# Performance work log

Measured on AMD Instinct MI355X. Metric: run time of the kernel, lower is better.

The kernel has to match this reference:

```python
import jax, jax.numpy as jnp
import numpy as np

B, T, F, H = 64, 512, 1024, 1024

def setup_inputs() -> dict:
    key = jax.random.key(0)
    ks = jax.random.split(key, 13)
    def w(k, shape):
        return jax.random.normal(k, shape, dtype=jnp.float32) * 0.02
    inp = {"x": jax.random.normal(ks[0], (B, T, F), dtype=jnp.float32)}
    names = ["i", "f", "g", "o"]
    for j, n in enumerate(names):
        inp[f"U_{n}"] = w(ks[1 + 3 * j], (F, H))
        inp[f"V_{n}"] = w(ks[2 + 3 * j], (H, H))
        inp[f"b_{n}"] = w(ks[3 + 3 * j], (H,))
    return inp


def reference(x, U_i, V_i, b_i, U_f, V_f, b_f, U_g, V_g, b_g, U_o, V_o, b_o):
    batch = x.shape[0]
    hid = V_i.shape[0]
    # Concatenate the 4 gate projections into single GEMMs (same math, fused).
    U = jnp.concatenate([U_i, U_f, U_g, U_o], axis=1)  # [F, 4H]
    V = jnp.concatenate([V_i, V_f, V_g, V_o], axis=1)  # [H, 4H]
    b = jnp.concatenate([b_i, b_f, b_g, b_o], axis=0)  # [4H]
    # Precompute input contribution for all timesteps in one big GEMM.
    xU = jnp.einsum("btf,fk->btk", x, U) + b           # [B, T, 4H]
    xU_t = jnp.swapaxes(xU, 0, 1)                       # [T, B, 4H]

    def step(carry, xu):
        h, c = carry
        z = xu + h @ V                                  # [B, 4H]
        zi, zf, zg, zo = jnp.split(z, 4, axis=-1)
        i_t = jax.nn.sigmoid(zi)
        f_t = jax.nn.sigmoid(zf)
        g_t = jnp.tanh(zg)
        o_t = jnp.tanh(zo)  # NOTE: source uses tanh (not sigmoid) for output gate
        c = f_t * c + i_t * g_t
        h = o_t * jnp.tanh(c)
        return (h, c), None

    h0 = jnp.zeros((batch, hid), dtype=x.dtype)
    c0 = jnp.zeros((batch, hid), dtype=x.dtype)
    (h_t, c_t), _ = jax.lax.scan(step, (h0, c0), xU_t)
    return h_t
```

## Files before the change

### kernel.cpp

```cpp
#include <hip/hip_runtime.h>

using u16 = unsigned short;
using u32 = unsigned int;
using u64 = unsigned long long;
using bf16x8 = __attribute__((ext_vector_type(8))) short;
using f16x8  = __attribute__((ext_vector_type(8))) _Float16;
using f32x4  = __attribute__((ext_vector_type(4))) float;
using u32x4  = __attribute__((ext_vector_type(4))) unsigned int;

static constexpr size_t XU_OFF = 0;
static constexpr size_t XU_BYTES = (size_t)512 * 64 * 4096 * 2;
static constexpr size_t XB_OFF = XU_OFF + XU_BYTES;
static constexpr size_t XB_BYTES = (size_t)64 * 512 * 1024 * 2;
static constexpr size_t UT_OFF = XB_OFF + XB_BYTES;
static constexpr size_t WT_BYTES = (size_t)4096 * 1024 * 2;
static constexpr size_t VT_OFF = UT_OFF + WT_BYTES;
static constexpr size_t BP_OFF = VT_OFF + WT_BYTES;
static constexpr size_t BP_BYTES = 4096 * 4;
static constexpr size_t HT_PLANE = (size_t)2 * 4 * 16 * 1024 * 2;
static constexpr size_t HHI_OFF = BP_OFF + BP_BYTES;
static constexpr size_t HLO_OFF = HHI_OFF + HT_PLANE;
static constexpr size_t FLAG_OFF = HLO_OFF + HT_PLANE;
static constexpr size_t FLAG_BYTES = 4096;

__device__ __forceinline__ float bf2f(u32 u) {
    return __uint_as_float(u << 16);
}
__device__ __forceinline__ u16 f2bf(float f) {
    u32 u = __float_as_uint(f);
    u32 r = (u + 0x7FFFu + ((u >> 16) & 1u)) >> 16;
    return (u16)r;
}
__device__ __forceinline__ u16 f2h(float f) {
    _Float16 x = (_Float16)f;
    union { _Float16 h; u16 u; } cv;
    cv.h = x;
    return cv.u;
}

__device__ __forceinline__ float fast_sigmoid(float x) {
    return __builtin_amdgcn_rcpf(1.f + __expf(-x));
}
__device__ __forceinline__ float fast_tanh(float x) {
    return 1.f - 2.f * __builtin_amdgcn_rcpf(1.f + __expf(2.f * x));
}

__device__ __forceinline__ u32x4 load16_uc(const u16* p) {
    u32x4 v;
    asm volatile("global_load_dwordx4 %0, %1, off sc0 sc1"
                 : "=v"(v)
                 : "v"(p));
    return v;
}

__device__ __forceinline__ void wait_vm4(int j, u32x4& a) {
    switch (j) {
    case 0:  asm volatile("s_waitcnt vmcnt(3)" : "+v"(a)); break;
    case 1:  asm volatile("s_waitcnt vmcnt(2)" : "+v"(a)); break;
    case 2:  asm volatile("s_waitcnt vmcnt(1)" : "+v"(a)); break;
    default: asm volatile("s_waitcnt vmcnt(0)" : "+v"(a)); break;
    }
}

__device__ __forceinline__ void gld16(const u16* g, u16* l) {
    __builtin_amdgcn_global_load_lds((const __attribute__((address_space(1))) void*)g,
                                     (__attribute__((address_space(3))) void*)l,
                                     16, 0, 0);
}

__global__ void cvt_x_kernel(const float4* __restrict__ x, uint2* __restrict__ xb) {
    int i = blockIdx.x * 256 + threadIdx.x;
#pragma unroll
    for (int k = 0; k < 8; ++k) {
        int idx = i + k * 1048576;
        float4 v = x[idx];
        uint2 o;
        o.x = (u32)f2bf(v.x) | ((u32)f2bf(v.y) << 16);
        o.y = (u32)f2bf(v.z) | ((u32)f2bf(v.w) << 16);
        xb[idx] = o;
    }
}

__global__ void repack_kernel(const float* U0, const float* U1, const float* U2, const float* U3,
                              const float* V0, const float* V1, const float* V2, const float* V3,
                              u16* UT, u16* VT) {
    __shared__ u16 tile[64][65];
    int bx  = blockIdx.x;
    int mat = bx >> 8;
    int rem = bx & 255;
    int tf = rem >> 4, th = rem & 15;
    int f0 = tf * 64, h0 = th * 64;
    const float* srcs[8] = {U0, U1, U2, U3, V0, V1, V2, V3};
    const float* s = srcs[mat];
    u16* d = (mat < 4) ? UT : VT;
    bool isU = (mat < 4);
    int g = mat & 3;
    int c = threadIdx.x & 63;
    int r = threadIdx.x >> 6;
#pragma unroll
    for (int i = 0; i < 16; ++i) {
        int fr = r + i * 4;
        float v = s[(size_t)(f0 + fr) * 1024 + h0 + c];
        tile[fr][c] = isU ? f2bf(v) : f2h(v);
    }
    __syncthreads();
#pragma unroll
    for (int i = 0; i < 16; ++i) {
        int hcl = r + i * 4;
        d[(size_t)((h0 + hcl) * 4 + g) * 1024 + f0 + c] = tile[c][hcl];
    }
}

__global__ void bias_kernel(const float* b0, const float* b1, const float* b2, const float* b3,
                            float* bp) {
    int n = blockIdx.x * 256 + threadIdx.x;
    int g = n & 3, hc = n >> 2;
    const float* bs[4] = {b0, b1, b2, b3};
    bp[n] = bs[g][hc];
}

__global__ void __launch_bounds__(256) gemm_xu_kernel(const u16* __restrict__ xb,
                                                      const u16* __restrict__ UT,
                                                      const float* __restrict__ bp,
                                                      u16* __restrict__ xu) {
    __shared__ u16 As[128 * 32];
    __shared__ u16 Bs[128 * 32];

    int bx0 = blockIdx.x;
    int bx = (bx0 & 7) * 1024 + (bx0 >> 3);
    int nt = bx & 31, mt = bx >> 5;
    int tid = threadIdx.x;
    int lane = tid & 63, wv = tid >> 6;
    int wm = wv & 1, wn = wv >> 1;
    int l15 = lane & 15, quad = lane >> 4;

    int idr = tid >> 2, idk = (tid & 3) * 8;
    const u16* aSrc0 = xb + (size_t)(mt * 128 + idr) * 1024 + idk;
    const u16* aSrc1 = aSrc0 + (size_t)64 * 1024;
    const u16* bSrc0 = UT + (size_t)(nt * 128 + idr) * 1024 + idk;
    const u16* bSrc1 = bSrc0 + (size_t)64 * 1024;
    u16* aDst0 = As + (size_t)tid * 8;
    u16* aDst1 = As + (size_t)(tid + 256) * 8;
    u16* bDst0 = Bs + (size_t)tid * 8;
    u16* bDst1 = Bs + (size_t)(tid + 256) * 8;

    int arow = wm * 64 + l15;
    int brow = wn * 64 + l15;
    int brow0 = nt * 128 + brow;

    f32x4 acc[4][4];
#pragma unroll
    for (int i = 0; i < 4; ++i)
#pragma unroll
        for (int j = 0; j < 4; ++j) acc[i][j] = f32x4{0.f, 0.f, 0.f, 0.f};

    float biasv[4];
#pragma unroll
    for (int j = 0; j < 4; ++j) biasv[j] = bp[brow0 + 16 * j];

    for (int k0 = 0; k0 < 1024; k0 += 32) {
        gld16(aSrc0 + k0, aDst0);
        gld16(aSrc1 + k0, aDst1);
        gld16(bSrc0 + k0, bDst0);
        gld16(bSrc1 + k0, bDst1);
        __syncthreads();

        bf16x8 af[4], bfv[4];
#pragma unroll
        for (int i = 0; i < 4; ++i)
            af[i] = *(const bf16x8*)(As + (size_t)(arow + i * 16) * 32 + quad * 8);
#pragma unroll
        for (int j = 0; j < 4; ++j)
            bfv[j] = *(const bf16x8*)(Bs + (size_t)(brow + j * 16) * 32 + quad * 8);
#pragma unroll
        for (int i = 0; i < 4; ++i)
#pragma unroll
            for (int j = 0; j < 4; ++j)
                acc[i][j] = __builtin_amdgcn_mfma_f32_16x16x32_bf16(af[i], bfv[j], acc[i][j], 0, 0, 0);
        __syncthreads();
    }

#pragma unroll
    for (int i = 0; i < 4; ++i) {
        int rbase = mt * 128 + wm * 64 + 16 * i + quad * 4;
#pragma unroll
        for (int j = 0; j < 4; ++j) {
            int col = brow0 + 16 * j;
            float bj = biasv[j];
#pragma unroll
            for (int rg = 0; rg < 4; ++rg) {
                int r = rbase + rg;
                int b_i = r >> 9, t_i = r & 511;
                xu[((size_t)(t_i * 64 + b_i) << 12) + col] = f2bf(acc[i][j][rg] + bj);
            }
        }
    }
}

__global__ void __launch_bounds__(512, 2) lstm_rec_kernel(const u16* __restrict__ xu,
                                                          const u16* __restrict__ VT,
                                                          u16* hhi,
                                                          u16* hlo,
                                                          u32* flags,
                                                          float* __restrict__ out) {
    __shared__ float zs[8][16][132];

    int bx = blockIdx.x;
    int g  = bx & 3;
    int cb = bx >> 2;
    int tid = threadIdx.x;
    int lane = tid & 63, wv = tid >> 6;
    int l15 = lane & 15, quad = lane >> 4;
    int r  = tid >> 5;
    int hc = tid & 31;

    f16x8 vfrag[8][4];
    {
        const u16* vb = VT + ((size_t)(cb * 128 + l15) * 1024) + wv * 128 + quad * 8;
#pragma unroll
        for (int nt = 0; nt < 8; ++nt)
#pragma unroll
            for (int j = 0; j < 4; ++j)
                vfrag[nt][j] = *(const f16x8*)(vb + (size_t)nt * 16 * 1024 + j * 32);
    }

    u32* gflags = flags + g * 64;
    int myp = 4 * wv + (lane & 3);

    float c = 0.f;
    float h = 0.f;

    uint2 xraw = *(const uint2*)(xu + ((size_t)(g * 16 + r) << 12) + cb * 128 + hc * 4);

    for (int t = 0; t < 512; ++t) {
        f32x4 acc[8];
#pragma unroll
        for (int nt = 0; nt < 8; ++nt) acc[nt] = f32x4{0.f, 0.f, 0.f, 0.f};

        if (t) {
            for (;;) {
                u32 f = __hip_atomic_load(gflags + myp, __ATOMIC_RELAXED,
                                          __HIP_MEMORY_SCOPE_AGENT);
                if (__ballot(f >= (u32)t) == ~0ull) break;
                __builtin_amdgcn_s_sleep(1);
            }
            asm volatile("" ::: "memory");

            const u16* hB = hhi + (((size_t)(t & 1) * 4 + g) * 16 + l15) * 1024
                          + wv * 128 + quad * 8;
            u32x4 hv[4];
#pragma unroll
            for (int j = 0; j < 4; ++j)
                hv[j] = load16_uc(hB + j * 32);
#pragma unroll
            for (int j = 0; j < 4; ++j) {
                wait_vm4(j, hv[j]);
                union { u32x4 q; f16x8 v; } ah;
                ah.q = hv[j];
#pragma unroll
                for (int nt = 0; nt < 8; ++nt)
                    acc[nt] = __builtin_amdgcn_mfma_f32_16x16x32_f16(ah.v, vfrag[nt][j], acc[nt], 0, 0, 0);
            }
        }

#pragma unroll
        for (int nt = 0; nt < 8; ++nt)
#pragma unroll
            for (int rg = 0; rg < 4; ++rg)
                zs[wv][quad * 4 + rg][nt * 16 + l15] = acc[nt][rg];
        __syncthreads();

        float4 s = {0.f, 0.f, 0.f, 0.f};
#pragma unroll
        for (int w = 0; w < 8; ++w) {
            float4 v = *(const float4*)&zs[w][r][hc * 4];
            s.x += v.x; s.y += v.y; s.z += v.z; s.w += v.w;
        }
        float z0 = s.x + bf2f(xraw.x & 0xFFFFu);
        float z1 = s.y + bf2f(xraw.x >> 16);
        float z2 = s.z + bf2f(xraw.y & 0xFFFFu);
        float z3 = s.w + bf2f(xraw.y >> 16);

        float it_ = fast_sigmoid(z0);
        float ft_ = fast_sigmoid(z1);
        float gt_ = fast_tanh(z2);
        float ot_ = fast_tanh(z3);
        c = ft_ * c + it_ * gt_;
        h = ot_ * fast_tanh(c);

        if (t == 511) break;

        size_t sidx = (((size_t)((t + 1) & 1) * 4 + g) * 16 + r) * 1024 + cb * 32 + hc;
        __hip_atomic_store(hhi + sidx, f2h(h), __ATOMIC_RELAXED,
                           __HIP_MEMORY_SCOPE_AGENT);
        asm volatile("s_waitcnt vmcnt(0)" ::: "memory");
        __syncthreads();
        if (tid == 0)
            __hip_atomic_store(gflags + cb, (u32)(t + 1), __ATOMIC_RELAXED,
                               __HIP_MEMORY_SCOPE_AGENT);

        xraw = *(const uint2*)(xu + ((size_t)((t + 1) * 64 + g * 16 + r) << 12) + cb * 128 + hc * 4);
    }

    out[(size_t)(g * 16 + r) * 1024 + cb * 32 + hc] = h;
}

extern "C" void kernel_launch(void* const* d_in, const int* in_sizes, int n_in,
                              void* d_out, int out_size, void* d_ws, size_t ws_size,
                              hipStream_t stream) {
    char* ws = (char*)d_ws;
    const float* x = (const float*)d_in[0];
    const float *U[4], *V[4], *b[4];
    for (int g = 0; g < 4; ++g) {
        U[g] = (const float*)d_in[1 + 3 * g];
        V[g] = (const float*)d_in[2 + 3 * g];
        b[g] = (const float*)d_in[3 + 3 * g];
    }
    u16*   xu = (u16*)(ws + XU_OFF);
    u16*   xb = (u16*)(ws + XB_OFF);
    u16*   UT = (u16*)(ws + UT_OFF);
    u16*   VT = (u16*)(ws + VT_OFF);
    float* bp = (float*)(ws + BP_OFF);
    u16*   hhi = (u16*)(ws + HHI_OFF);
    u16*   hlo = (u16*)(ws + HLO_OFF);
    u32*   flags = (u32*)(ws + FLAG_OFF);
    float* out = (float*)d_out;

    hipMemsetAsync(ws + FLAG_OFF, 0, FLAG_BYTES, stream);

    cvt_x_kernel<<<4096, 256, 0, stream>>>((const float4*)x, (uint2*)xb);
    repack_kernel<<<2048, 256, 0, stream>>>(U[0], U[1], U[2], U[3],
                                            V[0], V[1], V[2], V[3], UT, VT);
    bias_kernel<<<16, 256, 0, stream>>>(b[0], b[1], b[2], b[3], bp);
    gemm_xu_kernel<<<8192, 256, 0, stream>>>(xb, UT, bp, xu);

    void* args[] = {(void*)&xu, (void*)&VT, (void*)&hhi, (void*)&hlo,
                    (void*)&flags, (void*)&out};
    hipLaunchCooperativeKernel((const void*)lstm_rec_kernel, dim3(128), dim3(512),
                               args, 0, stream);
}
```

Baseline: 2.222 ms.

## Fuse input-projection GEMM into recurrent kernel and overlap it with recurrence

Replaces the separate xU GEMM launch with a cooperative fused kernel of 256 blocks. Every block first computes 8 GEMM tiles, which covers the first time chunk. The 128 extra blocks then produce the remaining time chunks in the background while the 128 recurrent blocks consume them, gated by per-chunk atomic counters. GEMM output is staged through LDS and written with 16-byte write-through stores, and the unused hlo buffer is removed. The aim is to hide most of the GEMM behind the latency-bound recurrence. The risks are a smaller 128x64-per-wave-split GEMM tile, lower occupancy from the larger LDS footprint, and recurrent blocks stalling if producers fall behind.

```diff
diff --git a/kernel.cpp b/kernel.cpp
--- a/kernel.cpp
+++ b/kernel.cpp
@@ -19,8 +19,7 @@
 static constexpr size_t BP_BYTES = 4096 * 4;
 static constexpr size_t HT_PLANE = (size_t)2 * 4 * 16 * 1024 * 2;
 static constexpr size_t HHI_OFF = BP_OFF + BP_BYTES;
-static constexpr size_t HLO_OFF = HHI_OFF + HT_PLANE;
-static constexpr size_t FLAG_OFF = HLO_OFF + HT_PLANE;
+static constexpr size_t FLAG_OFF = HHI_OFF + HT_PLANE;
 static constexpr size_t FLAG_BYTES = 4096;
 
 __device__ __forceinline__ float bf2f(u32 u) {
@@ -53,6 +52,11 @@
     return v;
 }
 
+__device__ __forceinline__ void store16_wt(u16* p, u32x4 v) {
+    asm volatile("global_store_dwordx4 %0, %1, off sc0 sc1"
+                 :: "v"(p), "v"(v) : "memory");
+}
+
 __device__ __forceinline__ void wait_vm4(int j, u32x4& a) {
     switch (j) {
     case 0:  asm volatile("s_waitcnt vmcnt(3)" : "+v"(a)); break;
@@ -66,6 +70,15 @@
     __builtin_amdgcn_global_load_lds((const __attribute__((address_space(1))) void*)g,
                                      (__attribute__((address_space(3))) void*)l,
                                      16, 0, 0);
+}
+
+__device__ __forceinline__ void wait_chunk(const u32* cnt, int c) {
+    for (;;) {
+        u32 v = __hip_atomic_load(cnt + c, __ATOMIC_RELAXED, __HIP_MEMORY_SCOPE_AGENT);
+        if (v >= 2048u) break;
+        __builtin_amdgcn_s_sleep(8);
+    }
+    asm volatile("" ::: "memory");
 }
 
 __global__ void cvt_x_kernel(const float4* __restrict__ x, uint2* __restrict__ xb) {
@@ -119,93 +132,99 @@
     bp[n] = bs[g][hc];
 }
 
-__global__ void __launch_bounds__(256) gemm_xu_kernel(const u16* __restrict__ xb,
-                                                      const u16* __restrict__ UT,
-                                                      const float* __restrict__ bp,
-                                                      u16* __restrict__ xu) {
+__device__ __forceinline__ void gemm_tile(int tau,
+        const u16* __restrict__ xb, const u16* __restrict__ UT,
+        const float* __restrict__ bp, u16* __restrict__ xu,
+        u16* As, u16* Bs, u16* Cs, u32* cnt) {
+    int tc = tau >> 11, rem = tau & 2047;
+    int b = rem >> 5, nt = rem & 31, mt = b * 4 + tc;
+    int tid = threadIdx.x;
+    int lane = tid & 63, wv = tid >> 6;
+    int wm = wv >> 2, wn = wv & 3;
+    int l15 = lane & 15, quad = lane >> 4;
+
+    int idr = tid >> 2, idk = (tid & 3) * 8;
+    const u16* aS = xb + (size_t)(mt * 128 + idr) * 1024 + idk;
+    const u16* bS = UT + (size_t)(nt * 128 + idr) * 1024 + idk;
+    u16* aD = As + (size_t)tid * 8;
+    u16* bD = Bs + (size_t)tid * 8;
+
+    f32x4 acc[4][2];
+#pragma unroll
+    for (int i = 0; i < 4; ++i)
+#pragma unroll
+        for (int j = 0; j < 2; ++j) acc[i][j] = f32x4{0.f, 0.f, 0.f, 0.f};
+
+    float biasv[2];
+#pragma unroll
+    for (int j = 0; j < 2; ++j) biasv[j] = bp[nt * 128 + wn * 32 + j * 16 + l15];
+
+    for (int k0 = 0; k0 < 1024; k0 += 32) {
+        gld16(aS + k0, aD);
+        gld16(bS + k0, bD);
+        __syncthreads();
+        bf16x8 af[4], bfv[2];
+#pragma unroll
+        for (int i = 0; i < 4; ++i)
+            af[i] = *(const bf16x8*)(As + (size_t)(wm * 64 + i * 16 + l15) * 32 + quad * 8);
+#pragma unroll
+        for (int j = 0; j < 2; ++j)
+            bfv[j] = *(const bf16x8*)(Bs + (size_t)(wn * 32 + j * 16 + l15) * 32 + quad * 8);
+#pragma unroll
+        for (int i = 0; i < 4; ++i)
+#pragma unroll
+            for (int j = 0; j < 2; ++j)
+                acc[i][j] = __builtin_amdgcn_mfma_f32_16x16x32_bf16(af[i], bfv[j], acc[i][j], 0, 0, 0);
+        __syncthreads();
+    }
+
+#pragma unroll
+    for (int i = 0; i < 4; ++i)
+#pragma unroll
+        for (int j = 0; j < 2; ++j)
+#pragma unroll
+            for (int rg = 0; rg < 4; ++rg)
+                Cs[(size_t)(wm * 64 + i * 16 + quad * 4 + rg) * 136 + wn * 32 + j * 16 + l15] =
+                    f2bf(acc[i][j][rg] + biasv[j]);
+    __syncthreads();
+
+#pragma unroll
+    for (int p = 0; p < 4; ++p) {
+        int id = p * 512 + tid;
+        int row = id >> 4, q = id & 15;
+        u32x4 v = *(const u32x4*)(Cs + (size_t)row * 136 + q * 8);
+        int gr = mt * 128 + row;
+        int t_i = gr & 511, b_i = gr >> 9;
+        store16_wt(xu + (((size_t)(t_i * 64 + b_i)) << 12) + nt * 128 + q * 8, v);
+    }
+    asm volatile("s_waitcnt vmcnt(0)" ::: "memory");
+    __syncthreads();
+    if (tid == 0)
+        __hip_atomic_fetch_add(cnt + tc, 1u, __ATOMIC_RELAXED, __HIP_MEMORY_SCOPE_AGENT);
+}
+
+__global__ void __launch_bounds__(512, 2) lstm_fused_kernel(
+        const u16* __restrict__ xb, const u16* __restrict__ UT,
+        const float* __restrict__ bp, u16* __restrict__ xu,
+        const u16* __restrict__ VT, u16* hhi, u32* flags, u32* cnt,
+        float* __restrict__ out) {
     __shared__ u16 As[128 * 32];
     __shared__ u16 Bs[128 * 32];
-
-    int bx0 = blockIdx.x;
-    int bx = (bx0 & 7) * 1024 + (bx0 >> 3);
-    int nt = bx & 31, mt = bx >> 5;
-    int tid = threadIdx.x;
-    int lane = tid & 63, wv = tid >> 6;
-    int wm = wv & 1, wn = wv >> 1;
-    int l15 = lane & 15, quad = lane >> 4;
-
-    int idr = tid >> 2, idk = (tid & 3) * 8;
-    const u16* aSrc0 = xb + (size_t)(mt * 128 + idr) * 1024 + idk;
-    const u16* aSrc1 = aSrc0 + (size_t)64 * 1024;
-    const u16* bSrc0 = UT + (size_t)(nt * 128 + idr) * 1024 + idk;
-    const u16* bSrc1 = bSrc0 + (size_t)64 * 1024;
-    u16* aDst0 = As + (size_t)tid * 8;
-    u16* aDst1 = As + (size_t)(tid + 256) * 8;
-    u16* bDst0 = Bs + (size_t)tid * 8;
-    u16* bDst1 = Bs + (size_t)(tid + 256) * 8;
-
-    int arow = wm * 64 + l15;
-    int brow = wn * 64 + l15;
-    int brow0 = nt * 128 + brow;
-
-    f32x4 acc[4][4];
-#pragma unroll
-    for (int i = 0; i < 4; ++i)
-#pragma unroll
-        for (int j = 0; j < 4; ++j) acc[i][j] = f32x4{0.f, 0.f, 0.f, 0.f};
-
-    float biasv[4];
-#pragma unroll
-    for (int j = 0; j < 4; ++j) biasv[j] = bp[brow0 + 16 * j];
-
-    for (int k0 = 0; k0 < 1024; k0 += 32) {
-        gld16(aSrc0 + k0, aDst0);
-        gld16(aSrc1 + k0, aDst1);
-        gld16(bSrc0 + k0, bDst0);
-        gld16(bSrc1 + k0, bDst1);
-        __syncthreads();
-
-        bf16x8 af[4], bfv[4];
-#pragma unroll
-        for (int i = 0; i < 4; ++i)
-            af[i] = *(const bf16x8*)(As + (size_t)(arow + i * 16) * 32 + quad * 8);
-#pragma unroll
-        for (int j = 0; j < 4; ++j)
-            bfv[j] = *(const bf16x8*)(Bs + (size_t)(brow + j * 16) * 32 + quad * 8);
-#pragma unroll
-        for (int i = 0; i < 4; ++i)
-#pragma unroll
-            for (int j = 0; j < 4; ++j)
-                acc[i][j] = __builtin_amdgcn_mfma_f32_16x16x32_bf16(af[i], bfv[j], acc[i][j], 0, 0, 0);
-        __syncthreads();
-    }
-
-#pragma unroll
-    for (int i = 0; i < 4; ++i) {
-        int rbase = mt * 128 + wm * 64 + 16 * i + quad * 4;
-#pragma unroll
-        for (int j = 0; j < 4; ++j) {
-            int col = brow0 + 16 * j;
-            float bj = biasv[j];
-#pragma unroll
-            for (int rg = 0; rg < 4; ++rg) {
-                int r = rbase + rg;
-                int b_i = r >> 9, t_i = r & 511;
-                xu[((size_t)(t_i * 64 + b_i) << 12) + col] = f2bf(acc[i][j][rg] + bj);
-            }
-        }
-    }
-}
-
-__global__ void __launch_bounds__(512, 2) lstm_rec_kernel(const u16* __restrict__ xu,
-                                                          const u16* __restrict__ VT,
-                                                          u16* hhi,
-                                                          u16* hlo,
-                                                          u32* flags,
-                                                          float* __restrict__ out) {
+    __shared__ u16 Cs[128 * 136];
     __shared__ float zs[8][16][132];
 
     int bx = blockIdx.x;
+
+    for (int p = 0; p < 8; ++p)
+        gemm_tile(bx * 8 + p, xb, UT, bp, xu, As, Bs, Cs, cnt);
+
+    if (bx >= 128) {
+        int gid = bx - 128;
+        for (int p = 0; p < 48; ++p)
+            gemm_tile(2048 + p * 128 + gid, xb, UT, bp, xu, As, Bs, Cs, cnt);
+        return;
+    }
+
     int g  = bx & 3;
     int cb = bx >> 2;
     int tid = threadIdx.x;
@@ -230,6 +249,7 @@
     float c = 0.f;
     float h = 0.f;
 
+    wait_chunk(cnt, 0);
     uint2 xraw = *(const uint2*)(xu + ((size_t)(g * 16 + r) << 12) + cb * 128 + hc * 4);
 
     for (int t = 0; t < 512; ++t) {
@@ -299,6 +319,7 @@
             __hip_atomic_store(gflags + cb, (u32)(t + 1), __ATOMIC_RELAXED,
                                __HIP_MEMORY_SCOPE_AGENT);
 
+        if (((t + 1) & 127) == 0) wait_chunk(cnt, (t + 1) >> 7);
         xraw = *(const uint2*)(xu + ((size_t)((t + 1) * 64 + g * 16 + r) << 12) + cb * 128 + hc * 4);
     }
 
@@ -322,8 +343,8 @@
     u16*   VT = (u16*)(ws + VT_OFF);
     float* bp = (float*)(ws + BP_OFF);
     u16*   hhi = (u16*)(ws + HHI_OFF);
-    u16*   hlo = (u16*)(ws + HLO_OFF);
     u32*   flags = (u32*)(ws + FLAG_OFF);
+    u32*   cnt = (u32*)(ws + FLAG_OFF + 2048);
     float* out = (float*)d_out;
 
     hipMemsetAsync(ws + FLAG_OFF, 0, FLAG_BYTES, stream);
@@ -332,10 +353,10 @@
     repack_kernel<<<2048, 256, 0, stream>>>(U[0], U[1], U[2], U[3],
                                             V[0], V[1], V[2], V[3], UT, VT);
     bias_kernel<<<16, 256, 0, stream>>>(b[0], b[1], b[2], b[3], bp);
-    gemm_xu_kernel<<<8192, 256, 0, stream>>>(xb, UT, bp, xu);
-
-    void* args[] = {(void*)&xu, (void*)&VT, (void*)&hhi, (void*)&hlo,
-                    (void*)&flags, (void*)&out};
-    hipLaunchCooperativeKernel((const void*)lstm_rec_kernel, dim3(128), dim3(512),
+
+    void* args[] = {(void*)&xb, (void*)&UT, (void*)&bp, (void*)&xu,
+                    (void*)&VT, (void*)&hhi, (void*)&flags, (void*)&cnt,
+                    (void*)&out};
+    hipLaunchCooperativeKernel((const void*)lstm_fused_kernel, dim3(256), dim3(512),
                                args, 0, stream);
 }
```

After: 2.192 ms. About the same (-1.3%).
